# Optimization experiments

Hardware: AMD Instinct MI355X
Metric: run time of the kernel (lower is better)

The kernel has to match this reference:

```python
import jax, jax.numpy as jnp
import numpy as np

B, N, M = 16, 4096, 1024
C_IN, C_SKIP, C_OUT = 256, 128, 256
K = 3
BN_EPS = 1e-5


def setup_inputs() -> dict:
    key = jax.random.key(0)
    ks = jax.random.split(key, 6)
    s1 = (6.0 / (C_IN + C_SKIP + C_OUT)) ** 0.5  # xavier-uniform bound, ~scale
    s2 = (6.0 / (2 * C_OUT)) ** 0.5
    return {
        "points": jax.random.normal(ks[0], (B, 3, N), jnp.float32),
        "point_features": jax.random.normal(ks[1], (B, C_SKIP, N), jnp.float32),
        "centroids": jax.random.normal(ks[2], (B, 3, M), jnp.float32),
        "centroid_features": jax.random.normal(ks[3], (B, C_IN, M), jnp.float32),
        "W1": jax.random.uniform(ks[4], (C_OUT, C_IN + C_SKIP), jnp.float32, -s1, s1),
        "b1": jnp.zeros((C_OUT,), jnp.float32),
        "gamma": jnp.ones((C_OUT,), jnp.float32),
        "beta": jnp.zeros((C_OUT,), jnp.float32),
        "W2": jax.random.uniform(ks[5], (C_OUT, C_OUT), jnp.float32, -s2, s2),
        "b2": jnp.zeros((C_OUT,), jnp.float32),
    }


def _knn_interpolate(x, pos_x, pos_y):
    # x: [B,M,C], pos_x: [B,M,3], pos_y: [B,N,3]. torch_geometric knn_interpolate, k=3.
    d2 = (jnp.sum(pos_y * pos_y, -1)[:, :, None]
          + jnp.sum(pos_x * pos_x, -1)[:, None, :]
          - 2.0 * jnp.einsum('bnd,bmd->bnm', pos_y, pos_x))  # [B,N,M]
    neg_vals, idx = jax.lax.top_k(-d2, K)                    # k smallest distances
    w = 1.0 / jnp.maximum(-neg_vals, 1e-16)                  # inverse-squared-distance weights
    # original computes indices/weights under torch.no_grad()
    idx = jax.lax.stop_gradient(idx)
    w = jax.lax.stop_gradient(w)
    xk = jax.vmap(lambda xb, ib: xb[ib])(x, idx)             # [B,N,K,C]
    return jnp.einsum('bnkc,bnk->bnc', xk, w) / jnp.sum(w, -1, keepdims=True)


def reference(points, point_features, centroids, centroid_features,
              W1, b1, gamma, beta, W2, b2):
    # Faithful to the original torch .reshape/.view calls on channel-first layout
    pos_y = points.reshape(-1, 3).reshape(B, N, 3)
    pos_x = centroids.reshape(-1, 3).reshape(B, M, 3)
    x = centroid_features.reshape(-1, C_IN).reshape(B, M, C_IN)
    interp = _knn_interpolate(x, pos_x, pos_y)               # [B,N,C_IN]
    interp = interp.reshape(-1, C_IN).reshape(B, C_IN, N)    # faithful .view(B, C, -1)
    h = jnp.concatenate([point_features, interp], axis=1)    # [B, C_SKIP+C_IN, N]
    # Conv1d(kernel=1) -> channel GEMM
    h = jnp.einsum('oc,bcn->bon', W1, h) + b1[None, :, None]
    # BatchNorm1d, training mode (biased batch var), eps=1e-5
    mean = jnp.mean(h, axis=(0, 2), keepdims=True)
    var = jnp.var(h, axis=(0, 2), keepdims=True)
    h = (h - mean) * jax.lax.rsqrt(var + BN_EPS) * gamma[None, :, None] + beta[None, :, None]
    h = jax.nn.relu(h)
    return jnp.einsum('oc,bcn->bon', W2, h) + b2[None, :, None]
```

## Files before the change

kernel.cpp:

```cpp
#include <hip/hip_runtime.h>

#define BB   16
#define NN   4096
#define MM   1024
#define CIN  256
#define CSK  128
#define COUT 256
#define KCH  384
#define NP   65536
#define NSEG2 512
#define NCHUNK 8
#define MCH  (MM / NCHUNK)
#define CVB  32

typedef __attribute__((ext_vector_type(8))) short bf16x8;
typedef __attribute__((ext_vector_type(4))) float f32x4;
typedef __attribute__((ext_vector_type(8))) unsigned short ushort8v;
typedef __attribute__((ext_vector_type(4))) unsigned short ushort4v;

static __device__ __forceinline__ unsigned short f2bf(float f) {
    unsigned u = __builtin_bit_cast(unsigned, f);
    u += 0x7fffu + ((u >> 16) & 1u);
    return (unsigned short)(u >> 16);
}
static __device__ __forceinline__ float bf2f(unsigned short h) {
    unsigned u = ((unsigned)h) << 16;
    return __builtin_bit_cast(float, u);
}

#define KSEL(d, m) do {                                                     \
    unsigned long long cc0, cc1, cc2;                                       \
    asm("v_cmp_lt_f32 %[c0], %[vd], %[vd0]\n\t"                             \
        "v_cmp_lt_f32 %[c1], %[vd], %[vd1]\n\t"                             \
        "v_cmp_lt_f32 %[c2], %[vd], %[vd2]\n\t"                             \
        "v_cndmask_b32 %[vi2], %[vi2], %[vm], %[c2]\n\t"                    \
        "v_cndmask_b32 %[vi2], %[vi2], %[vi1], %[c1]\n\t"                   \
        "v_cndmask_b32 %[vi1], %[vi1], %[vm], %[c1]\n\t"                    \
        "v_cndmask_b32 %[vi1], %[vi1], %[vi0], %[c0]\n\t"                   \
        "v_cndmask_b32 %[vi0], %[vi0], %[vm], %[c0]\n\t"                    \
        "v_med3_f32 %[vd2], %[vd], %[vd1], %[vd2]\n\t"                      \
        "v_med3_f32 %[vd1], %[vd], %[vd0], %[vd1]\n\t"                      \
        "v_min_f32 %[vd0], %[vd0], %[vd]"                                   \
        : [vd0]"+v"(d0), [vd1]"+v"(d1), [vd2]"+v"(d2v),                     \
          [vi0]"+v"(i0), [vi1]"+v"(i1), [vi2]"+v"(i2),                      \
          [c0]"=&s"(cc0), [c1]"=&s"(cc1), [c2]"=&s"(cc2)                    \
        : [vd]"v"(d), [vm]"v"(m));                                          \
} while (0)

__global__ __launch_bounds__(256) void megak_kernel(
    const float* __restrict__ pts, const float* __restrict__ cen,
    float* __restrict__ pdist, int* __restrict__ pidx,
    const float* __restrict__ cf, unsigned short* __restrict__ cfb,
    const float* __restrict__ pf, unsigned short* __restrict__ HbT,
    const float* __restrict__ W1, const float* __restrict__ W2,
    unsigned short* __restrict__ W1b, unsigned short* __restrict__ W2b)
{
    __shared__ union { float scw[MCH]; float ls[64][65]; } su;
    int blk = blockIdx.x;
    int t = threadIdx.x;

    if (blk < 2048) {
        int p0    = (blk >> 3) * 256;
        int chunk = blk & 7;
        int b     = p0 >> 12;
        int m0    = chunk * MCH;
        const float* cb = cen + (size_t)b * 3 * MM + 3 * m0;
        if (t < MCH) {
            float x = cb[3*t], y = cb[3*t+1], z = cb[3*t+2];
            su.scw[t] = x*x + y*y + z*z;
        }
        __syncthreads();

        int p = p0 + t;
        int n = p & (NN - 1);
        const float* pb = pts + (size_t)b * 3 * NN;
        float px = pb[3*n], py = pb[3*n+1], pz = pb[3*n+2];
        float pw = px*px + py*py + pz*pz;

        float d0 = 1e30f, d1 = 1e30f, d2v = 1e30f;
        int   i0 = 0, i1 = 0, i2 = 0;
        #pragma unroll 8
        for (int m = 0; m < MCH; ++m) {
            float cx = cb[3*m], cy = cb[3*m+1], cz = cb[3*m+2];
            float cw = su.scw[m];
            float dot = px*cx + py*cy + pz*cz;
            float d = (pw + cw) - 2.0f * dot;
            KSEL(d, m);
        }
        int base = (p * NCHUNK + chunk) * 3;
        pdist[base] = d0;      pdist[base+1] = d1;      pdist[base+2] = d2v;
        pidx[base]  = m0 + i0; pidx[base+1]  = m0 + i1; pidx[base+2]  = m0 + i2;
        return;
    }
    if (blk < 4096) {
        int g = blk - 2048;
        size_t e8 = ((size_t)g * 256 + t) * 8;
        const float4* cf4 = (const float4*)(cf + e8);
        float4 a = cf4[0], b4 = cf4[1];
        ushort8v w;
        w[0]=f2bf(a.x); w[1]=f2bf(a.y); w[2]=f2bf(a.z); w[3]=f2bf(a.w);
        w[4]=f2bf(b4.x); w[5]=f2bf(b4.y); w[6]=f2bf(b4.z); w[7]=f2bf(b4.w);
        *(ushort8v*)&cfb[e8] = w;
        return;
    }
    if (blk < 6144) {
        int g = blk - 4096;
        int b = g >> 7;
        int r = g & 127;
        int n0 = (r >> 1) * 64;
        int c0 = (r & 1) * 64;
        const float* src = pf + (size_t)b * CSK * NN;
        #pragma unroll
        for (int i = 0; i < 16; ++i) {
            int id = t + i * 256;
            int cc = id >> 6, nn = id & 63;
            su.ls[nn][cc] = src[(size_t)(c0 + cc) * NN + n0 + nn];
        }
        __syncthreads();
        int row = t & 63, ch0 = (t >> 6) * 16;
        unsigned short* dst = HbT + ((size_t)b * NN + n0 + row) * KCH + c0 + ch0;
        #pragma unroll
        for (int g2 = 0; g2 < 2; ++g2) {
            ushort8v w;
            #pragma unroll
            for (int j = 0; j < 8; ++j) w[j] = f2bf(su.ls[row][ch0 + g2*8 + j]);
            *(ushort8v*)&dst[g2*8] = w;
        }
        return;
    }
    {
        int i = (blk - 6144) * 256 + t;
        if (i < COUT * KCH) W1b[i] = f2bf(W1[i]);
        else {
            int j = i - COUT * KCH;
            if (j < COUT * COUT) W2b[j] = f2bf(W2[j]);
        }
    }
}

__global__ __launch_bounds__(256) void interp_kernel(
    const unsigned short* __restrict__ cfb, const float* __restrict__ pdist,
    const int* __restrict__ pidx, unsigned short* __restrict__ HbT)
{
    __shared__ int   li[CVB][3];
    __shared__ float lw[CVB][3];
    __shared__ unsigned short tile[CVB][258];
    int xcd = blockIdx.x & 7;
    int j   = blockIdx.x >> 3;
    int b   = xcd * 2 + (j >> 7);
    int rem = j & 127;
    int hi  = rem >> 3;
    int ch  = rem & 7;
    int t = threadIdx.x;
    if (t < CVB) {
        int P = b * NN + (ch * CVB + t) * 16 + hi;
        float d0 = 1e30f, d1 = 1e30f, d2v = 1e30f;
        int   i0 = 0, i1 = 0, i2 = 0;
        int base = P * NCHUNK * 3;
        #pragma unroll
        for (int c = 0; c < NCHUNK * 3; ++c) {
            float d = pdist[base + c];
            int   i = pidx[base + c];
            bool c2 = d < d2v, c1 = d < d1, c0 = d < d0;
            d2v = c1 ? d1 : (c2 ? d : d2v);
            i2  = c1 ? i1 : (c2 ? i : i2);
            d1  = c0 ? d0 : (c1 ? d : d1);
            i1  = c0 ? i0 : (c1 ? i : i1);
            d0  = c0 ? d  : d0;
            i0  = c0 ? i  : i0;
        }
        float w0 = 1.0f / fmaxf(d0,  1e-16f);
        float w1 = 1.0f / fmaxf(d1,  1e-16f);
        float w2 = 1.0f / fmaxf(d2v, 1e-16f);
        float inv = 1.0f / (w0 + w1 + w2);
        li[t][0] = i0;     li[t][1] = i1;     li[t][2] = i2;
        lw[t][0] = w0*inv; lw[t][1] = w1*inv; lw[t][2] = w2*inv;
    }
    __syncthreads();
    const unsigned short* cfbb = cfb + (size_t)b * MM * CIN;
    #pragma unroll 4
    for (int cv = 0; cv < CVB; ++cv) {
        float v = lw[cv][0] * bf2f(cfbb[(size_t)li[cv][0] * CIN + t])
                + lw[cv][1] * bf2f(cfbb[(size_t)li[cv][1] * CIN + t])
                + lw[cv][2] * bf2f(cfbb[(size_t)li[cv][2] * CIN + t]);
        tile[cv][t] = f2bf(v);
    }
    __syncthreads();
    size_t dstbase = ((size_t)b * NN + hi * 256 + t) * KCH + CSK + ch * CVB;
    #pragma unroll
    for (int g = 0; g < CVB / 8; ++g) {
        ushort8v w;
        #pragma unroll
        for (int j2 = 0; j2 < 8; ++j2) w[j2] = tile[g*8 + j2][t];
        *(ushort8v*)&HbT[dstbase + g*8] = w;
    }
}

#define SWZ(r) (((r) >> 1) & 3)
#define GLL(g, l) __builtin_amdgcn_global_load_lds(                          \
    (const __attribute__((address_space(1))) unsigned int*)(g),              \
    (__attribute__((address_space(3))) unsigned int*)(l), 16, 0, 0)

__global__ __launch_bounds__(256) void gemm1_kernel(
    const unsigned short* __restrict__ HbT, const unsigned short* __restrict__ W1b,
    const float* __restrict__ b1, unsigned short* __restrict__ h1T,
    float* __restrict__ psum, float* __restrict__ psq)
{
    __shared__ union {
        struct {
            __align__(16) unsigned short A[2][128 * 32];
            __align__(16) unsigned short B[2][128 * 32];
        } s;
        struct {
            __align__(16) unsigned short eps[64][136];
            float red[512];
        } e;
    } u;
    int pp0 = blockIdx.x * 128;
    int o0  = blockIdx.y * 128;
    int t = threadIdx.x;
    int wv = t >> 6, L = t & 63;
    int wr = wv >> 1, wc = wv & 1;
    int lr = L & 15, lk = L >> 4;

    const unsigned short* gA[2];
    const unsigned short* gB[2];
    int ldso[2];
    #pragma unroll
    for (int j = 0; j < 2; ++j) {
        int row = wv*32 + j*16 + (L >> 2);
        int sg  = (L & 3) ^ SWZ(row);
        gA[j] = W1b + (size_t)(o0 + row) * KCH + sg*8;
        gB[j] = HbT + (size_t)(pp0 + row) * KCH + sg*8;
        ldso[j] = wv*1024 + j*512;
    }
    int offA[4], offB[4];
    #pragma unroll
    for (int m = 0; m < 4; ++m) {
        int ar = wr*64 + m*16 + lr;
        offA[m] = ar*32 + (lk ^ SWZ(ar))*8;
    }
    #pragma unroll
    for (int n = 0; n < 4; ++n) {
        int br = wc*64 + n*16 + lr;
        offB[n] = br*32 + (lk ^ SWZ(br))*8;
    }

    f32x4 acc[4][4] = {};

    #pragma unroll
    for (int j = 0; j < 2; ++j) {
        GLL(gA[j], &u.s.A[0][ldso[j]]);
        GLL(gB[j], &u.s.B[0][ldso[j]]);
    }
    __syncthreads();

    for (int ks = 0; ks < KCH / 32; ++ks) {
        int cur = ks & 1;
        if (ks + 1 < KCH / 32) {
            #pragma unroll
            for (int j = 0; j < 2; ++j) {
                GLL(gA[j] + (ks + 1) * 32, &u.s.A[cur ^ 1][ldso[j]]);
                GLL(gB[j] + (ks + 1) * 32, &u.s.B[cur ^ 1][ldso[j]]);
            }
        }
        bf16x8 af[4], bfr[4];
        #pragma unroll
        for (int m = 0; m < 4; ++m) af[m] = *(const bf16x8*)&u.s.A[cur][offA[m]];
        #pragma unroll
        for (int n = 0; n < 4; ++n) bfr[n] = *(const bf16x8*)&u.s.B[cur][offB[n]];
        #pragma unroll
        for (int m = 0; m < 4; ++m)
            #pragma unroll
            for (int n = 0; n < 4; ++n)
                acc[m][n] = __builtin_amdgcn_mfma_f32_16x16x32_bf16(af[m], bfr[n], acc[m][n], 0, 0, 0);
        __syncthreads();
    }

    float bb[4][4];
    #pragma unroll
    for (int m = 0; m < 4; ++m)
        #pragma unroll
        for (int j = 0; j < 4; ++j)
            bb[m][j] = b1[o0 + wr*64 + m*16 + lk*4 + j];
    float sprt[4][4] = {{0.f}}, qprt[4][4] = {{0.f}};
    #pragma unroll
    for (int pw = 0; pw < 2; ++pw) {
        if (wc == pw) {
            #pragma unroll
            for (int n = 0; n < 4; ++n) {
                int r = n*16 + lr;
                #pragma unroll
                for (int m = 0; m < 4; ++m) {
                    f32x4 v = acc[m][n];
                    ushort4v w;
                    #pragma unroll
                    for (int j = 0; j < 4; ++j) {
                        float f = v[j] + bb[m][j];
                        w[j] = f2bf(f);
                        float rr = bf2f(w[j]);
                        sprt[m][j] += rr;
                        qprt[m][j] = fmaf(rr, rr, qprt[m][j]);
                    }
                    *(ushort4v*)&u.e.eps[r][wr*64 + m*16 + lk*4] = w;
                }
            }
        }
        __syncthreads();
        {
            int r = t >> 2, seg = t & 3;
            size_t gbase = ((size_t)(pp0 + pw*64 + r)) * COUT + o0 + seg * 32;
            #pragma unroll
            for (int k = 0; k < 4; ++k) {
                ushort8v vv = *(const ushort8v*)&u.e.eps[r][seg*32 + k*8];
                *(ushort8v*)&h1T[gbase + k*8] = vv;
            }
        }
        __syncthreads();
    }
    #pragma unroll
    for (int m = 0; m < 4; ++m)
        #pragma unroll
        for (int j = 0; j < 4; ++j) {
            float s = sprt[m][j], q = qprt[m][j];
            #pragma unroll
            for (int off = 1; off < 16; off <<= 1) {
                s += __shfl_xor(s, off, 64);
                q += __shfl_xor(q, off, 64);
            }
            sprt[m][j] = s; qprt[m][j] = q;
        }
    if (lr == 0) {
        #pragma unroll
        for (int m = 0; m < 4; ++m)
            #pragma unroll
            for (int j = 0; j < 4; ++j) {
                int ol = wr*64 + m*16 + lk*4 + j;
                u.e.red[wc*128 + ol]       = sprt[m][j];
                u.e.red[256 + wc*128 + ol] = qprt[m][j];
            }
    }
    __syncthreads();
    if (t < 128) {
        float S = u.e.red[t] + u.e.red[128 + t];
        float Q = u.e.red[256 + t] + u.e.red[384 + t];
        psum[(size_t)(o0 + t) * NSEG2 + blockIdx.x] = S;
        psq [(size_t)(o0 + t) * NSEG2 + blockIdx.x] = Q;
    }
}

__global__ __launch_bounds__(256) void bnfin_kernel(
    const float* __restrict__ psum, const float* __restrict__ psq,
    const float* __restrict__ gamma, const float* __restrict__ beta,
    float* __restrict__ bnscale, float* __restrict__ bnshift)
{
    __shared__ float rs[256], rq[256];
    int o = blockIdx.x, t = threadIdx.x;
    rs[t] = psum[(size_t)o * NSEG2 + t] + psum[(size_t)o * NSEG2 + 256 + t];
    rq[t] = psq [(size_t)o * NSEG2 + t] + psq [(size_t)o * NSEG2 + 256 + t];
    __syncthreads();
    for (int off = 128; off > 0; off >>= 1) {
        if (t < off) { rs[t] += rs[t + off]; rq[t] += rq[t + off]; }
        __syncthreads();
    }
    if (t == 0) {
        float mean = rs[0] * (1.0f / NP);
        float var  = rq[0] * (1.0f / NP) - mean * mean;
        float sc = gamma[o] * rsqrtf(var + 1e-5f);
        bnscale[o] = sc;
        bnshift[o] = fmaf(-mean, sc, beta[o]);
    }
}

__global__ __launch_bounds__(256) void gemm2_kernel(
    const unsigned short* __restrict__ h1T, const unsigned short* __restrict__ W2b,
    const float* __restrict__ b2, const float* __restrict__ bnscale,
    const float* __restrict__ bnshift, float* __restrict__ out)
{
    __shared__ union {
        struct {
            __align__(16) unsigned short As[128][40];
            __align__(16) unsigned short Bs[128][40];
        } s;
        float eps[64][132];
    } u;
    __shared__ float scs[COUT], shs[COUT];
    int pp0 = blockIdx.x * 128;
    int o0  = blockIdx.y * 128;
    int t = threadIdx.x;
    scs[t] = bnscale[t]; shs[t] = bnshift[t];
    int wid = t >> 6, lane = t & 63;
    int wr = wid >> 1, wc = wid & 1;
    int lr = lane & 15, lk = lane >> 4;

    int rowi[2], qi[2];
    ushort8v ra[2], rb[2];
    #pragma unroll
    for (int i = 0; i < 2; ++i) { int id = t + i*256; rowi[i] = id >> 2; qi[i] = id & 3; }
    #pragma unroll
    for (int i = 0; i < 2; ++i) {
        ra[i] = *(const ushort8v*)&W2b[(size_t)(o0 + rowi[i]) * COUT + qi[i]*8];
        rb[i] = *(const ushort8v*)&h1T[(size_t)(pp0 + rowi[i]) * COUT + qi[i]*8];
    }
    f32x4 acc[4][4] = {};
    __syncthreads();

    for (int c0 = 0; c0 < COUT; c0 += 32) {
        #pragma unroll
        for (int i = 0; i < 2; ++i) {
            *(ushort8v*)&u.s.As[rowi[i]][qi[i]*8] = ra[i];
            ushort8v bv;
            #pragma unroll
            for (int j = 0; j < 8; ++j) {
                float f = fmaf(bf2f(rb[i][j]), scs[c0 + qi[i]*8 + j], shs[c0 + qi[i]*8 + j]);
                bv[j] = f2bf(fmaxf(f, 0.0f));
            }
            *(ushort8v*)&u.s.Bs[rowi[i]][qi[i]*8] = bv;
        }
        __syncthreads();
        int cn = (c0 + 32 < COUT) ? c0 + 32 : c0;
        #pragma unroll
        for (int i = 0; i < 2; ++i) {
            ra[i] = *(const ushort8v*)&W2b[(size_t)(o0 + rowi[i]) * COUT + cn + qi[i]*8];
            rb[i] = *(const ushort8v*)&h1T[(size_t)(pp0 + rowi[i]) * COUT + cn + qi[i]*8];
        }
        bf16x8 af[4], bfr[4];
        #pragma unroll
        for (int m = 0; m < 4; ++m) af[m] = *(const bf16x8*)&u.s.As[wr*64 + m*16 + lr][lk*8];
        #pragma unroll
        for (int n = 0; n < 4; ++n) bfr[n] = *(const bf16x8*)&u.s.Bs[wc*64 + n*16 + lr][lk*8];
        #pragma unroll
        for (int m = 0; m < 4; ++m)
            #pragma unroll
            for (int n = 0; n < 4; ++n)
                acc[m][n] = __builtin_amdgcn_mfma_f32_16x16x32_bf16(af[m], bfr[n], acc[m][n], 0, 0, 0);
        __syncthreads();
    }
    int b  = pp0 >> 12;
    int n0 = pp0 & (NN - 1);
    float b2v[4][4];
    #pragma unroll
    for (int m = 0; m < 4; ++m)
        #pragma unroll
        for (int j = 0; j < 4; ++j)
            b2v[m][j] = b2[o0 + wr*64 + m*16 + lk*4 + j];
    #pragma unroll
    for (int ow = 0; ow < 2; ++ow) {
        if (wr == ow) {
            #pragma unroll
            for (int m = 0; m < 4; ++m)
                #pragma unroll
                for (int n = 0; n < 4; ++n) {
                    f32x4 v = acc[m][n];
                    int pl = wc*64 + n*16 + lr;
                    #pragma unroll
                    for (int j = 0; j < 4; ++j)
                        u.eps[m*16 + lk*4 + j][pl] = v[j] + b2v[m][j];
                }
        }
        __syncthreads();
        #pragma unroll
        for (int i = 0; i < 8; ++i) {
            int r  = (t >> 5) + i * 8;
            int c4 = (t & 31) * 4;
            float4 v = *(const float4*)&u.eps[r][c4];
            *(float4*)&out[((size_t)(b * COUT + o0 + ow*64 + r)) * NN + n0 + c4] = v;
        }
        __syncthreads();
    }
}

extern "C" void kernel_launch(void* const* d_in, const int* in_sizes, int n_in,
                              void* d_out, int out_size, void* d_ws, size_t ws_size,
                              hipStream_t stream)
{
    const float* pts   = (const float*)d_in[0];
    const float* pf    = (const float*)d_in[1];
    const float* cen   = (const float*)d_in[2];
    const float* cf    = (const float*)d_in[3];
    const float* W1    = (const float*)d_in[4];
    const float* b1    = (const float*)d_in[5];
    const float* gamma = (const float*)d_in[6];
    const float* beta  = (const float*)d_in[7];
    const float* W2    = (const float*)d_in[8];
    const float* b2    = (const float*)d_in[9];
    float* out = (float*)d_out;

    char* ws = (char*)d_ws;
    size_t off = 0;
    unsigned short* HbT = (unsigned short*)(ws + off); off += (size_t)NP * KCH * 2;
    unsigned short* h1T = (unsigned short*)(ws + off); off += (size_t)NP * COUT * 2;
    unsigned short* W1b = (unsigned short*)(ws + off); off += (size_t)COUT * KCH * 2;
    unsigned short* W2b = (unsigned short*)(ws + off); off += (size_t)COUT * COUT * 2;
    unsigned short* cfb = (unsigned short*)(ws + off); off += (size_t)BB * MM * CIN * 2;
    float* pdist   = (float*)(ws + off); off += (size_t)NP * NCHUNK * 3 * sizeof(float);
    int*   pidx    = (int*)(ws + off);   off += (size_t)NP * NCHUNK * 3 * sizeof(int);
    float* psum    = (float*)(ws + off); off += (size_t)COUT * NSEG2 * sizeof(float);
    float* psq     = (float*)(ws + off); off += (size_t)COUT * NSEG2 * sizeof(float);
    float* bnscale = (float*)(ws + off); off += 1024;
    float* bnshift = (float*)(ws + off); off += 1024;
    (void)ws_size; (void)in_sizes; (void)n_in; (void)out_size;

    hipLaunchKernelGGL(megak_kernel,  dim3(6784),         dim3(256), 0, stream,
                       pts, cen, pdist, pidx, cf, cfb, pf, HbT, W1, W2, W1b, W2b);
    hipLaunchKernelGGL(interp_kernel, dim3(2048),         dim3(256), 0, stream,
                       cfb, pdist, pidx, HbT);
    hipLaunchKernelGGL(gemm1_kernel,  dim3(NP / 128, 2),  dim3(256), 0, stream,
                       HbT, W1b, b1, h1T, psum, psq);
    hipLaunchKernelGGL(bnfin_kernel,  dim3(COUT),         dim3(256), 0, stream,
                       psum, psq, gamma, beta, bnscale, bnshift);
    hipLaunchKernelGGL(gemm2_kernel,  dim3(NP / 128, 2),  dim3(256), 0, stream,
                       h1T, W2b, b2, bnscale, bnshift, out);
}
```

Baseline: 132.5 us.

## Widen GEMM tiles to cover all output channels per block

Both channel GEMM kernels now use 512-thread blocks that compute all 256 output channels for a 128-point tile, instead of two 256-thread blocks each covering 128 channels. Each activation tile (HbT for gemm1, h1T for gemm2) is therefore loaded once rather than twice. In gemm2 this also halves the repeated BN+ReLU transform of the input tile. The cost is a grid of 512 blocks with more LDS per block, which may lower occupancy and leave CUs less evenly loaded.

```diff
diff --git a/kernel.cpp b/kernel.cpp
--- a/kernel.cpp
+++ b/kernel.cpp
@@ -201,68 +201,70 @@
     (const __attribute__((address_space(1))) unsigned int*)(g),              \
     (__attribute__((address_space(3))) unsigned int*)(l), 16, 0, 0)
 
-__global__ __launch_bounds__(256) void gemm1_kernel(
+__global__ __launch_bounds__(512) void gemm1_kernel(
     const unsigned short* __restrict__ HbT, const unsigned short* __restrict__ W1b,
     const float* __restrict__ b1, unsigned short* __restrict__ h1T,
     float* __restrict__ psum, float* __restrict__ psq)
 {
     __shared__ union {
         struct {
-            __align__(16) unsigned short A[2][128 * 32];
+            __align__(16) unsigned short A[2][256 * 32];
             __align__(16) unsigned short B[2][128 * 32];
         } s;
         struct {
-            __align__(16) unsigned short eps[64][136];
-            float red[512];
+            __align__(16) unsigned short eps[64][264];
+            float reds[512];
+            float redq[512];
         } e;
     } u;
     int pp0 = blockIdx.x * 128;
-    int o0  = blockIdx.y * 128;
     int t = threadIdx.x;
     int wv = t >> 6, L = t & 63;
-    int wr = wv >> 1, wc = wv & 1;
+    int wp = wv >> 2, wo = wv & 3;
     int lr = L & 15, lk = L >> 4;
 
     const unsigned short* gA[2];
-    const unsigned short* gB[2];
-    int ldso[2];
+    const unsigned short* gB;
+    int ldsoA[2], ldsoB;
     #pragma unroll
     for (int j = 0; j < 2; ++j) {
         int row = wv*32 + j*16 + (L >> 2);
         int sg  = (L & 3) ^ SWZ(row);
-        gA[j] = W1b + (size_t)(o0 + row) * KCH + sg*8;
-        gB[j] = HbT + (size_t)(pp0 + row) * KCH + sg*8;
-        ldso[j] = wv*1024 + j*512;
+        gA[j] = W1b + (size_t)row * KCH + sg*8;
+        ldsoA[j] = wv*1024 + j*512;
+    }
+    {
+        int row = wv*16 + (L >> 2);
+        int sg  = (L & 3) ^ SWZ(row);
+        gB = HbT + (size_t)(pp0 + row) * KCH + sg*8;
+        ldsoB = wv*512;
     }
     int offA[4], offB[4];
     #pragma unroll
     for (int m = 0; m < 4; ++m) {
-        int ar = wr*64 + m*16 + lr;
+        int ar = wo*64 + m*16 + lr;
         offA[m] = ar*32 + (lk ^ SWZ(ar))*8;
     }
     #pragma unroll
     for (int n = 0; n < 4; ++n) {
-        int br = wc*64 + n*16 + lr;
+        int br = wp*64 + n*16 + lr;
         offB[n] = br*32 + (lk ^ SWZ(br))*8;
     }
 
     f32x4 acc[4][4] = {};
 
     #pragma unroll
-    for (int j = 0; j < 2; ++j) {
-        GLL(gA[j], &u.s.A[0][ldso[j]]);
-        GLL(gB[j], &u.s.B[0][ldso[j]]);
-    }
+    for (int j = 0; j < 2; ++j) GLL(gA[j], &u.s.A[0][ldsoA[j]]);
+    GLL(gB, &u.s.B[0][ldsoB]);
     __syncthreads();
 
     for (int ks = 0; ks < KCH / 32; ++ks) {
         int cur = ks & 1;
         if (ks + 1 < KCH / 32) {
             #pragma unroll
-            for (int j = 0; j < 2; ++j) {
-                GLL(gA[j] + (ks + 1) * 32, &u.s.A[cur ^ 1][ldso[j]]);
-                GLL(gB[j] + (ks + 1) * 32, &u.s.B[cur ^ 1][ldso[j]]);
-            }
+            for (int j = 0; j < 2; ++j)
+                GLL(gA[j] + (ks + 1) * 32, &u.s.A[cur ^ 1][ldsoA[j]]);
+            GLL(gB + (ks + 1) * 32, &u.s.B[cur ^ 1][ldsoB]);
         }
         bf16x8 af[4], bfr[4];
         #pragma unroll
@@ -282,11 +284,11 @@
     for (int m = 0; m < 4; ++m)
         #pragma unroll
         for (int j = 0; j < 4; ++j)
-            bb[m][j] = b1[o0 + wr*64 + m*16 + lk*4 + j];
+            bb[m][j] = b1[wo*64 + m*16 + lk*4 + j];
     float sprt[4][4] = {{0.f}}, qprt[4][4] = {{0.f}};
     #pragma unroll
     for (int pw = 0; pw < 2; ++pw) {
-        if (wc == pw) {
+        if (wp == pw) {
             #pragma unroll
             for (int n = 0; n < 4; ++n) {
                 int r = n*16 + lr;
@@ -302,17 +304,17 @@
                         sprt[m][j] += rr;
                         qprt[m][j] = fmaf(rr, rr, qprt[m][j]);
                     }
-                    *(ushort4v*)&u.e.eps[r][wr*64 + m*16 + lk*4] = w;
+                    *(ushort4v*)&u.e.eps[r][wo*64 + m*16 + lk*4] = w;
                 }
             }
         }
         __syncthreads();
         {
-            int r = t >> 2, seg = t & 3;
-            size_t gbase = ((size_t)(pp0 + pw*64 + r)) * COUT + o0 + seg * 32;
+            int r = t >> 3, sg = t & 7;
+            size_t gbase = ((size_t)(pp0 + pw*64 + r)) * COUT + sg * 32;
             #pragma unroll
             for (int k = 0; k < 4; ++k) {
-                ushort8v vv = *(const ushort8v*)&u.e.eps[r][seg*32 + k*8];
+                ushort8v vv = *(const ushort8v*)&u.e.eps[r][sg*32 + k*8];
                 *(ushort8v*)&h1T[gbase + k*8] = vv;
             }
         }
@@ -335,17 +337,17 @@
         for (int m = 0; m < 4; ++m)
             #pragma unroll
             for (int j = 0; j < 4; ++j) {
-                int ol = wr*64 + m*16 + lk*4 + j;
-                u.e.red[wc*128 + ol]       = sprt[m][j];
-                u.e.red[256 + wc*128 + ol] = qprt[m][j];
+                int o = wo*64 + m*16 + lk*4 + j;
+                u.e.reds[wp*256 + o] = sprt[m][j];
+                u.e.redq[wp*256 + o] = qprt[m][j];
             }
     }
     __syncthreads();
-    if (t < 128) {
-        float S = u.e.red[t] + u.e.red[128 + t];
-        float Q = u.e.red[256 + t] + u.e.red[384 + t];
-        psum[(size_t)(o0 + t) * NSEG2 + blockIdx.x] = S;
-        psq [(size_t)(o0 + t) * NSEG2 + blockIdx.x] = Q;
+    if (t < 256) {
+        float S = u.e.reds[t] + u.e.reds[256 + t];
+        float Q = u.e.redq[t] + u.e.redq[256 + t];
+        psum[(size_t)t * NSEG2 + blockIdx.x] = S;
+        psq [(size_t)t * NSEG2 + blockIdx.x] = Q;
     }
 }
 
@@ -372,63 +374,57 @@
     }
 }
 
-__global__ __launch_bounds__(256) void gemm2_kernel(
+__global__ __launch_bounds__(512) void gemm2_kernel(
     const unsigned short* __restrict__ h1T, const unsigned short* __restrict__ W2b,
     const float* __restrict__ b2, const float* __restrict__ bnscale,
     const float* __restrict__ bnshift, float* __restrict__ out)
 {
     __shared__ union {
         struct {
-            __align__(16) unsigned short As[128][40];
+            __align__(16) unsigned short As[256][40];
             __align__(16) unsigned short Bs[128][40];
         } s;
         float eps[64][132];
     } u;
     __shared__ float scs[COUT], shs[COUT];
     int pp0 = blockIdx.x * 128;
-    int o0  = blockIdx.y * 128;
     int t = threadIdx.x;
-    scs[t] = bnscale[t]; shs[t] = bnshift[t];
-    int wid = t >> 6, lane = t & 63;
-    int wr = wid >> 1, wc = wid & 1;
-    int lr = lane & 15, lk = lane >> 4;
-
-    int rowi[2], qi[2];
-    ushort8v ra[2], rb[2];
-    #pragma unroll
-    for (int i = 0; i < 2; ++i) { int id = t + i*256; rowi[i] = id >> 2; qi[i] = id & 3; }
-    #pragma unroll
-    for (int i = 0; i < 2; ++i) {
-        ra[i] = *(const ushort8v*)&W2b[(size_t)(o0 + rowi[i]) * COUT + qi[i]*8];
-        rb[i] = *(const ushort8v*)&h1T[(size_t)(pp0 + rowi[i]) * COUT + qi[i]*8];
-    }
+    if (t < 256) { scs[t] = bnscale[t]; shs[t] = bnshift[t]; }
+    int wv = t >> 6, L = t & 63;
+    int wp = wv >> 2, wo = wv & 3;
+    int lr = L & 15, lk = L >> 4;
+
+    int arow = t >> 1, aq = (t & 1) * 16;
+    int brow = t >> 2, bq = (t & 3) * 8;
+    ushort8v ra0, ra1, rbv;
+    ra0 = *(const ushort8v*)&W2b[(size_t)arow * COUT + aq];
+    ra1 = *(const ushort8v*)&W2b[(size_t)arow * COUT + aq + 8];
+    rbv = *(const ushort8v*)&h1T[(size_t)(pp0 + brow) * COUT + bq];
     f32x4 acc[4][4] = {};
     __syncthreads();
 
     for (int c0 = 0; c0 < COUT; c0 += 32) {
-        #pragma unroll
-        for (int i = 0; i < 2; ++i) {
-            *(ushort8v*)&u.s.As[rowi[i]][qi[i]*8] = ra[i];
+        *(ushort8v*)&u.s.As[arow][aq]     = ra0;
+        *(ushort8v*)&u.s.As[arow][aq + 8] = ra1;
+        {
             ushort8v bv;
             #pragma unroll
             for (int j = 0; j < 8; ++j) {
-                float f = fmaf(bf2f(rb[i][j]), scs[c0 + qi[i]*8 + j], shs[c0 + qi[i]*8 + j]);
+                float f = fmaf(bf2f(rbv[j]), scs[c0 + bq + j], shs[c0 + bq + j]);
                 bv[j] = f2bf(fmaxf(f, 0.0f));
             }
-            *(ushort8v*)&u.s.Bs[rowi[i]][qi[i]*8] = bv;
+            *(ushort8v*)&u.s.Bs[brow][bq] = bv;
         }
         __syncthreads();
         int cn = (c0 + 32 < COUT) ? c0 + 32 : c0;
-        #pragma unroll
-        for (int i = 0; i < 2; ++i) {
-            ra[i] = *(const ushort8v*)&W2b[(size_t)(o0 + rowi[i]) * COUT + cn + qi[i]*8];
-            rb[i] = *(const ushort8v*)&h1T[(size_t)(pp0 + rowi[i]) * COUT + cn + qi[i]*8];
-        }
+        ra0 = *(const ushort8v*)&W2b[(size_t)arow * COUT + cn + aq];
+        ra1 = *(const ushort8v*)&W2b[(size_t)arow * COUT + cn + aq + 8];
+        rbv = *(const ushort8v*)&h1T[(size_t)(pp0 + brow) * COUT + cn + bq];
         bf16x8 af[4], bfr[4];
         #pragma unroll
-        for (int m = 0; m < 4; ++m) af[m] = *(const bf16x8*)&u.s.As[wr*64 + m*16 + lr][lk*8];
-        #pragma unroll
-        for (int n = 0; n < 4; ++n) bfr[n] = *(const bf16x8*)&u.s.Bs[wc*64 + n*16 + lr][lk*8];
+        for (int m = 0; m < 4; ++m) af[m] = *(const bf16x8*)&u.s.As[wo*64 + m*16 + lr][lk*8];
+        #pragma unroll
+        for (int n = 0; n < 4; ++n) bfr[n] = *(const bf16x8*)&u.s.Bs[wp*64 + n*16 + lr][lk*8];
         #pragma unroll
         for (int m = 0; m < 4; ++m)
             #pragma unroll
@@ -443,28 +439,31 @@
     for (int m = 0; m < 4; ++m)
         #pragma unroll
         for (int j = 0; j < 4; ++j)
-            b2v[m][j] = b2[o0 + wr*64 + m*16 + lk*4 + j];
-    #pragma unroll
-    for (int ow = 0; ow < 2; ++ow) {
-        if (wr == ow) {
+            b2v[m][j] = b2[wo*64 + m*16 + lk*4 + j];
+    #pragma unroll
+    for (int ow = 0; ow < 4; ++ow) {
+        if (wo == ow) {
             #pragma unroll
             for (int m = 0; m < 4; ++m)
                 #pragma unroll
                 for (int n = 0; n < 4; ++n) {
                     f32x4 v = acc[m][n];
-                    int pl = wc*64 + n*16 + lr;
+                    int pl = wp*64 + n*16 + lr;
                     #pragma unroll
                     for (int j = 0; j < 4; ++j)
                         u.eps[m*16 + lk*4 + j][pl] = v[j] + b2v[m][j];
                 }
         }
         __syncthreads();
-        #pragma unroll
-        for (int i = 0; i < 8; ++i) {
-            int r  = (t >> 5) + i * 8;
-            int c4 = (t & 31) * 4;
-            float4 v = *(const float4*)&u.eps[r][c4];
-            *(float4*)&out[((size_t)(b * COUT + o0 + ow*64 + r)) * NN + n0 + c4] = v;
+        {
+            int r  = t >> 3;
+            int c8 = (t & 7) * 16;
+            float* dst = out + ((size_t)(b * COUT + ow*64 + r)) * NN + n0 + c8;
+            #pragma unroll
+            for (int k = 0; k < 4; ++k) {
+                float4 v = *(const float4*)&u.eps[r][c8 + k*4];
+                *(float4*)&dst[k*4] = v;
+            }
         }
         __syncthreads();
     }
@@ -501,14 +500,14 @@
     float* bnshift = (float*)(ws + off); off += 1024;
     (void)ws_size; (void)in_sizes; (void)n_in; (void)out_size;
 
-    hipLaunchKernelGGL(megak_kernel,  dim3(6784),         dim3(256), 0, stream,
+    hipLaunchKernelGGL(megak_kernel,  dim3(6784),  dim3(256), 0, stream,
                        pts, cen, pdist, pidx, cf, cfb, pf, HbT, W1, W2, W1b, W2b);
-    hipLaunchKernelGGL(interp_kernel, dim3(2048),         dim3(256), 0, stream,
+    hipLaunchKernelGGL(interp_kernel, dim3(2048),  dim3(256), 0, stream,
                        cfb, pdist, pidx, HbT);
-    hipLaunchKernelGGL(gemm1_kernel,  dim3(NP / 128, 2),  dim3(256), 0, stream,
+    hipLaunchKernelGGL(gemm1_kernel,  dim3(512),   dim3(512), 0, stream,
                        HbT, W1b, b1, h1T, psum, psq);
-    hipLaunchKernelGGL(bnfin_kernel,  dim3(COUT),         dim3(256), 0, stream,
+    hipLaunchKernelGGL(bnfin_kernel,  dim3(COUT),  dim3(256), 0, stream,
                        psum, psq, gamma, beta, bnscale, bnshift);
-    hipLaunchKernelGGL(gemm2_kernel,  dim3(NP / 128, 2),  dim3(256), 0, stream,
+    hipLaunchKernelGGL(gemm2_kernel,  dim3(512),   dim3(512), 0, stream,
                        h1T, W2b, b2, bnscale, bnshift, out);
 }
```

Measured after the change: 138.2 us. +4.4%, slower.

## Restructure gemm1 to load MFMA fragments directly from global without LDS staging

Applied to the files above, without the earlier changes.

gemm1 no longer stages A/B tiles in double-buffered LDS via global_load_lds. Each wave now reads its bf16 fragments straight from global memory (relying on L1/L2 caching), and the per-k-step barriers are removed. The block is widened to 512 threads covering all 256 output channels for 128 points, so the grid becomes 512 blocks and the BN partial stats are written for every channel per block. This drops LDS traffic and syncs, but each wave issues uncoalesced 16-byte global loads with rows strided by KCH, and it gives up the cross-wave reuse that the shared tiles provided.

```diff
diff --git a/kernel.cpp b/kernel.cpp
--- a/kernel.cpp
+++ b/kernel.cpp
@@ -196,85 +196,45 @@
     }
 }
 
-#define SWZ(r) (((r) >> 1) & 3)
-#define GLL(g, l) __builtin_amdgcn_global_load_lds(                          \
-    (const __attribute__((address_space(1))) unsigned int*)(g),              \
-    (__attribute__((address_space(3))) unsigned int*)(l), 16, 0, 0)
-
-__global__ __launch_bounds__(256) void gemm1_kernel(
+__global__ __launch_bounds__(512) void gemm1_kernel(
     const unsigned short* __restrict__ HbT, const unsigned short* __restrict__ W1b,
     const float* __restrict__ b1, unsigned short* __restrict__ h1T,
     float* __restrict__ psum, float* __restrict__ psq)
 {
-    __shared__ union {
-        struct {
-            __align__(16) unsigned short A[2][128 * 32];
-            __align__(16) unsigned short B[2][128 * 32];
-        } s;
-        struct {
-            __align__(16) unsigned short eps[64][136];
-            float red[512];
-        } e;
-    } u;
+    __shared__ struct {
+        __align__(16) unsigned short eps[64][264];
+        float reds[512];
+        float redq[512];
+    } e;
     int pp0 = blockIdx.x * 128;
-    int o0  = blockIdx.y * 128;
     int t = threadIdx.x;
     int wv = t >> 6, L = t & 63;
-    int wr = wv >> 1, wc = wv & 1;
+    int wp = wv >> 2, wo = wv & 3;
     int lr = L & 15, lk = L >> 4;
 
-    const unsigned short* gA[2];
-    const unsigned short* gB[2];
-    int ldso[2];
-    #pragma unroll
-    for (int j = 0; j < 2; ++j) {
-        int row = wv*32 + j*16 + (L >> 2);
-        int sg  = (L & 3) ^ SWZ(row);
-        gA[j] = W1b + (size_t)(o0 + row) * KCH + sg*8;
-        gB[j] = HbT + (size_t)(pp0 + row) * KCH + sg*8;
-        ldso[j] = wv*1024 + j*512;
-    }
-    int offA[4], offB[4];
-    #pragma unroll
-    for (int m = 0; m < 4; ++m) {
-        int ar = wr*64 + m*16 + lr;
-        offA[m] = ar*32 + (lk ^ SWZ(ar))*8;
-    }
-    #pragma unroll
-    for (int n = 0; n < 4; ++n) {
-        int br = wc*64 + n*16 + lr;
-        offB[n] = br*32 + (lk ^ SWZ(br))*8;
-    }
+    const unsigned short* pA[4];
+    const unsigned short* pB[4];
+    #pragma unroll
+    for (int m = 0; m < 4; ++m)
+        pA[m] = W1b + (size_t)(wo*64 + m*16 + lr) * KCH + lk*8;
+    #pragma unroll
+    for (int n = 0; n < 4; ++n)
+        pB[n] = HbT + (size_t)(pp0 + wp*64 + n*16 + lr) * KCH + lk*8;
 
     f32x4 acc[4][4] = {};
 
-    #pragma unroll
-    for (int j = 0; j < 2; ++j) {
-        GLL(gA[j], &u.s.A[0][ldso[j]]);
-        GLL(gB[j], &u.s.B[0][ldso[j]]);
-    }
-    __syncthreads();
-
-    for (int ks = 0; ks < KCH / 32; ++ks) {
-        int cur = ks & 1;
-        if (ks + 1 < KCH / 32) {
-            #pragma unroll
-            for (int j = 0; j < 2; ++j) {
-                GLL(gA[j] + (ks + 1) * 32, &u.s.A[cur ^ 1][ldso[j]]);
-                GLL(gB[j] + (ks + 1) * 32, &u.s.B[cur ^ 1][ldso[j]]);
-            }
-        }
+    #pragma unroll 4
+    for (int c0 = 0; c0 < KCH; c0 += 32) {
         bf16x8 af[4], bfr[4];
         #pragma unroll
-        for (int m = 0; m < 4; ++m) af[m] = *(const bf16x8*)&u.s.A[cur][offA[m]];
-        #pragma unroll
-        for (int n = 0; n < 4; ++n) bfr[n] = *(const bf16x8*)&u.s.B[cur][offB[n]];
+        for (int m = 0; m < 4; ++m) af[m] = *(const bf16x8*)(pA[m] + c0);
+        #pragma unroll
+        for (int n = 0; n < 4; ++n) bfr[n] = *(const bf16x8*)(pB[n] + c0);
         #pragma unroll
         for (int m = 0; m < 4; ++m)
             #pragma unroll
             for (int n = 0; n < 4; ++n)
                 acc[m][n] = __builtin_amdgcn_mfma_f32_16x16x32_bf16(af[m], bfr[n], acc[m][n], 0, 0, 0);
-        __syncthreads();
     }
 
     float bb[4][4];
@@ -282,11 +242,11 @@
     for (int m = 0; m < 4; ++m)
         #pragma unroll
         for (int j = 0; j < 4; ++j)
-            bb[m][j] = b1[o0 + wr*64 + m*16 + lk*4 + j];
+            bb[m][j] = b1[wo*64 + m*16 + lk*4 + j];
     float sprt[4][4] = {{0.f}}, qprt[4][4] = {{0.f}};
     #pragma unroll
     for (int pw = 0; pw < 2; ++pw) {
-        if (wc == pw) {
+        if (wp == pw) {
             #pragma unroll
             for (int n = 0; n < 4; ++n) {
                 int r = n*16 + lr;
@@ -302,17 +262,17 @@
                         sprt[m][j] += rr;
                         qprt[m][j] = fmaf(rr, rr, qprt[m][j]);
                     }
-                    *(ushort4v*)&u.e.eps[r][wr*64 + m*16 + lk*4] = w;
+                    *(ushort4v*)&e.eps[r][wo*64 + m*16 + lk*4] = w;
                 }
             }
         }
         __syncthreads();
         {
-            int r = t >> 2, seg = t & 3;
-            size_t gbase = ((size_t)(pp0 + pw*64 + r)) * COUT + o0 + seg * 32;
+            int r = t >> 3, sg = t & 7;
+            size_t gbase = ((size_t)(pp0 + pw*64 + r)) * COUT + sg * 32;
             #pragma unroll
             for (int k = 0; k < 4; ++k) {
-                ushort8v vv = *(const ushort8v*)&u.e.eps[r][seg*32 + k*8];
+                ushort8v vv = *(const ushort8v*)&e.eps[r][sg*32 + k*8];
                 *(ushort8v*)&h1T[gbase + k*8] = vv;
             }
         }
@@ -335,17 +295,17 @@
         for (int m = 0; m < 4; ++m)
             #pragma unroll
             for (int j = 0; j < 4; ++j) {
-                int ol = wr*64 + m*16 + lk*4 + j;
-                u.e.red[wc*128 + ol]       = sprt[m][j];
-                u.e.red[256 + wc*128 + ol] = qprt[m][j];
+                int o = wo*64 + m*16 + lk*4 + j;
+                e.reds[wp*256 + o] = sprt[m][j];
+                e.redq[wp*256 + o] = qprt[m][j];
             }
     }
     __syncthreads();
-    if (t < 128) {
-        float S = u.e.red[t] + u.e.red[128 + t];
-        float Q = u.e.red[256 + t] + u.e.red[384 + t];
-        psum[(size_t)(o0 + t) * NSEG2 + blockIdx.x] = S;
-        psq [(size_t)(o0 + t) * NSEG2 + blockIdx.x] = Q;
+    if (t < 256) {
+        float S = e.reds[t] + e.reds[256 + t];
+        float Q = e.redq[t] + e.redq[256 + t];
+        psum[(size_t)t * NSEG2 + blockIdx.x] = S;
+        psq [(size_t)t * NSEG2 + blockIdx.x] = Q;
     }
 }
 
@@ -505,7 +465,7 @@
                        pts, cen, pdist, pidx, cf, cfb, pf, HbT, W1, W2, W1b, W2b);
     hipLaunchKernelGGL(interp_kernel, dim3(2048),         dim3(256), 0, stream,
                        cfb, pdist, pidx, HbT);
-    hipLaunchKernelGGL(gemm1_kernel,  dim3(NP / 128, 2),  dim3(256), 0, stream,
+    hipLaunchKernelGGL(gemm1_kernel,  dim3(512),          dim3(512), 0, stream,
                        HbT, W1b, b1, h1T, psum, psq);
     hipLaunchKernelGGL(bnfin_kernel,  dim3(COUT),         dim3(256), 0, stream,
                        psum, psq, gamma, beta, bnscale, bnshift);
```

Result: slower. 157.5 us (+18.9%).
